# Kernel optimization log

Hardware: AMD Instinct MI355X
Metric: run time of the kernel (lower is better)

## Reference

```python
import jax, jax.numpy as jnp
import numpy as np

N = 100000
E = 1600000
IN_DIM = 64
HID = 64
OUT = 64
NCLS = 40
EPS_BN = 1e-5


def _sym_norms(src, dst, n):
    # DGL GraphConv norm='both': src scaled by out_degree^-1/2, dst by in_degree^-1/2,
    # degrees clamped to min 1.
    ones = jnp.ones(src.shape[0], dtype=jnp.float32)
    deg_out = jax.ops.segment_sum(ones, src, num_segments=n)
    deg_in = jax.ops.segment_sum(ones, dst, num_segments=n)
    return jnp.clip(deg_out, 1.0) ** -0.5, jnp.clip(deg_in, 1.0) ** -0.5


def _graph_conv(x, src, dst, norm_src, norm_dst, W, b):
    # D_dst^{-1/2} A D_src^{-1/2} X W + b
    x = x * norm_src[:, None]
    agg = jax.ops.segment_sum(x[src], dst, num_segments=x.shape[0])
    agg = agg * norm_dst[:, None]
    return agg @ W + b


def _gcn(x, src, dst, W1, b1, W2, b2):
    ns, nd = _sym_norms(src, dst, x.shape[0])
    h = jax.nn.relu(_graph_conv(x, src, dst, ns, nd, W1, b1))
    return _graph_conv(h, src, dst, ns, nd, W2, b2)


def setup_inputs() -> dict:
    key = jax.random.key(0)
    ks = jax.random.split(key, 16)
    glorot = lambda k, fi, fo: jax.random.normal(k, (fi, fo), jnp.float32) * np.sqrt(2.0 / (fi + fo))
    return {
        "feat1": jax.random.normal(ks[0], (N, IN_DIM), jnp.float32),
        "src1": jax.random.randint(ks[1], (E,), 0, N, jnp.int32),
        "dst1": jax.random.randint(ks[2], (E,), 0, N, jnp.int32),
        "feat2": jax.random.normal(ks[3], (N, IN_DIM), jnp.float32),
        "src2": jax.random.randint(ks[4], (E,), 0, N, jnp.int32),
        "dst2": jax.random.randint(ks[5], (E,), 0, N, jnp.int32),
        "W1a": glorot(ks[6], IN_DIM, HID), "b1a": jnp.zeros(HID, jnp.float32),
        "W1b": glorot(ks[7], HID, OUT), "b1b": jnp.zeros(OUT, jnp.float32),
        "W2a": glorot(ks[8], IN_DIM, HID), "b2a": jnp.zeros(HID, jnp.float32),
        "W2b": glorot(ks[9], HID, OUT), "b2b": jnp.zeros(OUT, jnp.float32),
        "Wm1": glorot(ks[10], OUT, HID), "bm1": jnp.zeros(HID, jnp.float32),
        "gamma": jnp.ones(HID, jnp.float32), "beta": jnp.zeros(HID, jnp.float32),
        "Wm2": glorot(ks[11], HID, NCLS), "bm2": jnp.zeros(NCLS, jnp.float32),
    }


def reference(feat1, src1, dst1, feat2, src2, dst2,
              W1a, b1a, W1b, b1b, W2a, b2a, W2b, b2b,
              Wm1, bm1, gamma, beta, Wm2, bm2):
    h1 = _gcn(feat1, src1, dst1, W1a, b1a, W1b, b1b)
    h2 = _gcn(feat2, src2, dst2, W2a, b2a, W2b, b2b)
    # torch .std() is unbiased (ddof=1)
    z1 = (h1 - h1.mean(0)) / jnp.std(h1, axis=0, ddof=1)
    z2 = (h2 - h2.mean(0)) / jnp.std(h2, axis=0, ddof=1)
    z = (z1 + z2) * 0.5
    # MLP2 head: Linear -> BatchNorm1d (training-mode batch stats) -> ReLU -> Linear
    y = z @ Wm1 + bm1
    mu = y.mean(0)
    var = y.var(0)  # biased, as BN uses
    y = (y - mu) * jax.lax.rsqrt(var + EPS_BN) * gamma + beta
    pred_y = jax.nn.relu(y) @ Wm2 + bm2
    return (z1, z2, pred_y)
```

## Files before the change

### kernel.cpp

```cpp
#include <hip/hip_runtime.h>
#include <hip/hip_bf16.h>

#define DIM 64
#define NCLS_OUT 40
#define BSH 8
#define BROWS 256
#define BIN_CHUNK 12288

typedef __hip_bfloat16 bf16;

__device__ __forceinline__ float lane_bcast(float v, int l) {
  return __int_as_float(__builtin_amdgcn_readlane(__float_as_int(v), l));
}
__device__ __forceinline__ unsigned short f2bf_bits(float f) {
  bf16 h = __float2bfloat16(f);
  return *reinterpret_cast<unsigned short*>(&h);
}

__device__ __forceinline__ float ldf(const void* p, long i, int m) {
  return m ? ((const float*)p)[i] : __bfloat162float(((const bf16*)p)[i]);
}
__device__ __forceinline__ void stf(void* p, long i, float v, int m) {
  if (m) ((float*)p)[i] = v;
  else ((bf16*)p)[i] = __float2bfloat16(v);
}

__global__ void k_detect(const unsigned int* __restrict__ wds, int nw, int* __restrict__ mode) {
  __shared__ int cnt_s;
  if (threadIdx.x == 0) cnt_s = 0;
  __syncthreads();
  int c = 0;
  for (int i = threadIdx.x; i < nw; i += 1024) {
    unsigned h = wds[i] & 0xFFFFu;
    unsigned e = (h >> 7) & 0xFFu;
    if (e == 0xFFu || (e != 0u && e < 0x60u)) c++;
  }
  atomicAdd(&cnt_s, c);
  __syncthreads();
  if (threadIdx.x == 0) *mode = (cnt_s > nw / 16) ? 1 : 0;
}

__global__ void k_deg_out(const int* __restrict__ src1, const int* __restrict__ src2,
                          int* __restrict__ deg, int n, int e1, int etot) {
  int i = blockIdx.x * 256 + threadIdx.x;
  if (i >= etot) return;
  if (i < e1) atomicAdd(&deg[2 * n + src1[i]], 1);
  else atomicAdd(&deg[3 * n + src2[i - e1]], 1);
}

__global__ void k_norm(const int* __restrict__ deg, float* __restrict__ nrm, int n4) {
  int i = blockIdx.x * 256 + threadIdx.x;
  if (i < n4) {
    int d = deg[i];
    if (d < 1) d = 1;
    nrm[i] = rsqrtf((float)d);
  }
}

__global__ void k_bhist(const int* __restrict__ dst1, const int* __restrict__ dst2,
                        int* __restrict__ bh, int n, int e1, int etot, int NB) {
  extern __shared__ int cnt[];
  for (int b = threadIdx.x; b < NB; b += blockDim.x) cnt[b] = 0;
  __syncthreads();
  int stride = gridDim.x * blockDim.x;
  for (int i = blockIdx.x * blockDim.x + threadIdx.x; i < etot; i += stride) {
    int row = (i < e1) ? dst1[i] : (n + dst2[i - e1]);
    atomicAdd(&cnt[row >> BSH], 1);
  }
  __syncthreads();
  for (int b = threadIdx.x; b < NB; b += blockDim.x)
    if (cnt[b]) atomicAdd(&bh[b], cnt[b]);
}

__global__ void k_bscan(const int* __restrict__ bh, int* __restrict__ bbase,
                        int* __restrict__ gcur, int* __restrict__ rp,
                        int NB, int etot, int n2) {
  __shared__ int sm[256];
  __shared__ int carry_s;
  int t = threadIdx.x;
  if (t == 0) carry_s = 0;
  __syncthreads();
  for (int base = 0; base < NB; base += 256) {
    int i = base + t;
    int v = (i < NB) ? bh[i] : 0;
    sm[t] = v;
    __syncthreads();
    for (int o = 1; o < 256; o <<= 1) {
      int a = (t >= o) ? sm[t - o] : 0;
      __syncthreads();
      sm[t] += a;
      __syncthreads();
    }
    int c = carry_s;
    int excl = c + sm[t] - v;
    int tot = sm[255];
    __syncthreads();
    if (i < NB) { bbase[i] = excl; gcur[i] = excl; }
    if (t == 0) carry_s = c + tot;
    __syncthreads();
  }
  if (t == 0) { bbase[NB] = etot; rp[n2] = etot; }
}

__global__ void __launch_bounds__(256) k_bin(
    const int* __restrict__ src1, const int* __restrict__ dst1,
    const int* __restrict__ src2, const int* __restrict__ dst2,
    int* __restrict__ gcur, unsigned* __restrict__ eb,
    int n, int e1, int etot, int NB) {
  extern __shared__ int lds[];
  int* cnt = lds;
  int* base = lds + NB;
  int t = threadIdx.x;
  int c0 = blockIdx.x * BIN_CHUNK;
  int cend = c0 + BIN_CHUNK;
  if (cend > etot) cend = etot;
  for (int b = t; b < NB; b += 256) cnt[b] = 0;
  __syncthreads();
  for (int i = c0 + t; i < cend; i += 256) {
    int row = (i < e1) ? dst1[i] : (n + dst2[i - e1]);
    atomicAdd(&cnt[row >> BSH], 1);
  }
  __syncthreads();
  for (int b = t; b < NB; b += 256) {
    int c = cnt[b];
    base[b] = c ? atomicAdd(&gcur[b], c) : 0;
    cnt[b] = 0;
  }
  __syncthreads();
  for (int i = c0 + t; i < cend; i += 256) {
    int s, row;
    if (i < e1) { s = src1[i]; row = dst1[i]; }
    else { s = src2[i - e1]; row = n + dst2[i - e1]; }
    int b = row >> BSH;
    int l = atomicAdd(&cnt[b], 1);
    eb[base[b] + l] = ((unsigned)(row & (BROWS - 1)) << 24) | (unsigned)s;
  }
}

__global__ void __launch_bounds__(256) k_fine(
    const unsigned* __restrict__ eb, const int* __restrict__ bbase,
    int* __restrict__ rp, int* __restrict__ deg, int* __restrict__ sb,
    int n2, int NB) {
  __shared__ int hist[256];
  __shared__ int sm[256];
  __shared__ int curs[256];
  int t = threadIdx.x;
  for (int b = blockIdx.x; b < NB; b += gridDim.x) {
    int ebeg = bbase[b], eend = bbase[b + 1];
    hist[t] = 0;
    __syncthreads();
    for (int i = ebeg + t; i < eend; i += 256)
      atomicAdd(&hist[eb[i] >> 24], 1);
    __syncthreads();
    int v = hist[t];
    sm[t] = v;
    __syncthreads();
    for (int o = 1; o < 256; o <<= 1) {
      int a = (t >= o) ? sm[t - o] : 0;
      __syncthreads();
      sm[t] += a;
      __syncthreads();
    }
    int excl = sm[t] - v;
    int row = (b << BSH) + t;
    if (row < n2) { deg[row] = v; rp[row] = ebeg + excl; }
    curs[t] = excl;
    __syncthreads();
    for (int i = ebeg + t; i < eend; i += 256) {
      unsigned u = eb[i];
      int l = atomicAdd(&curs[u >> 24], 1);
      sb[ebeg + l] = (int)(u & 0xFFFFFFu);
    }
    __syncthreads();
  }
}

__global__ void k_scale_all(const void* __restrict__ f1, const void* __restrict__ f2,
                            const float* __restrict__ norms, bf16* __restrict__ P,
                            int n, const int* __restrict__ mode) {
  int m = *mode;
  int i = blockIdx.x * 256 + threadIdx.x;
  int nd = n * DIM;
  if (i >= 2 * nd) return;
  int g = i >= nd;
  int li = g ? i - nd : i;
  float ns = norms[2 * n + g * n + (li >> 6)];
  P[i] = __float2bfloat16(ldf(g ? f2 : f1, li, m) * ns);
}

__global__ void k_scale_one(const void* __restrict__ f, const float* __restrict__ ns,
                            bf16* __restrict__ P, int nd, const int* __restrict__ mode) {
  int m = *mode;
  int i = blockIdx.x * 256 + threadIdx.x;
  if (i < nd) P[i] = __float2bfloat16(ldf(f, i, m) * ns[i >> 6]);
}

__global__ void __launch_bounds__(256) k_gmm(
    const bf16* __restrict__ X, const int* __restrict__ rp, const int* __restrict__ sb,
    const void* __restrict__ Wg0, const void* __restrict__ bg0,
    const void* __restrict__ Wg1, const void* __restrict__ bg1,
    const float* __restrict__ pre0, const float* __restrict__ pre1,
    const float* __restrict__ post0, const float* __restrict__ post1,
    bf16* __restrict__ Y, int n, int relu, const int* __restrict__ mode,
    int dual, int gsel, float* __restrict__ stats) {
  int m = *mode;
  int t = threadIdx.x, lane = t & 63, wid = t >> 6;
  int g = dual ? (blockIdx.x & 1) : gsel;
  int ord = dual ? (blockIdx.x >> 1) : blockIdx.x;
  int nblk = dual ? (gridDim.x >> 1) : gridDim.x;
  int rowbase = dual ? g * n : 0;

  const void* W = g ? Wg1 : Wg0;
  const void* bb = g ? bg1 : bg0;
  const float* pre = g ? pre1 : pre0;
  const float* post = g ? post1 : post0;

  unsigned wp[32];
#pragma unroll
  for (int i = 0; i < 32; ++i) {
    unsigned lb = f2bf_bits(ldf(W, (2 * i) * 64 + lane, m));
    unsigned hb = f2bf_bits(ldf(W, (2 * i + 1) * 64 + lane, m));
    wp[i] = lb | (hb << 16);
  }
  float bias = ldf(bb, lane, m);
  float ps = 0.f, pq = 0.f;

  int stride = nblk * 4;
  for (int node = ord * 4 + wid; node < n; node += stride) {
    int b0 = rp[g * n + node], e0 = rp[g * n + node + 1];
    float a0 = 0.f, a1 = 0.f, a2 = 0.f, a3 = 0.f;
    for (int base = b0; base < e0; base += 64) {
      int cnt = e0 - base;
      if (cnt > 64) cnt = 64;
      int eidx = (lane < cnt) ? sb[base + lane] : 0;
      int j = 0;
      for (; j + 8 <= cnt; j += 8) {
        int s0 = __builtin_amdgcn_readlane(eidx, j);
        int s1 = __builtin_amdgcn_readlane(eidx, j + 1);
        int s2 = __builtin_amdgcn_readlane(eidx, j + 2);
        int s3 = __builtin_amdgcn_readlane(eidx, j + 3);
        int s4 = __builtin_amdgcn_readlane(eidx, j + 4);
        int s5 = __builtin_amdgcn_readlane(eidx, j + 5);
        int s6 = __builtin_amdgcn_readlane(eidx, j + 6);
        int s7 = __builtin_amdgcn_readlane(eidx, j + 7);
        float v0 = __bfloat162float(X[(long)(rowbase + s0) * DIM + lane]);
        float v1 = __bfloat162float(X[(long)(rowbase + s1) * DIM + lane]);
        float v2 = __bfloat162float(X[(long)(rowbase + s2) * DIM + lane]);
        float v3 = __bfloat162float(X[(long)(rowbase + s3) * DIM + lane]);
        float v4 = __bfloat162float(X[(long)(rowbase + s4) * DIM + lane]);
        float v5 = __bfloat162float(X[(long)(rowbase + s5) * DIM + lane]);
        float v6 = __bfloat162float(X[(long)(rowbase + s6) * DIM + lane]);
        float v7 = __bfloat162float(X[(long)(rowbase + s7) * DIM + lane]);
        a0 += v0; a1 += v1; a2 += v2; a3 += v3;
        a0 += v4; a1 += v5; a2 += v6; a3 += v7;
      }
      for (; j + 4 <= cnt; j += 4) {
        int s0 = __builtin_amdgcn_readlane(eidx, j);
        int s1 = __builtin_amdgcn_readlane(eidx, j + 1);
        int s2 = __builtin_amdgcn_readlane(eidx, j + 2);
        int s3 = __builtin_amdgcn_readlane(eidx, j + 3);
        a0 += __bfloat162float(X[(long)(rowbase + s0) * DIM + lane]);
        a1 += __bfloat162float(X[(long)(rowbase + s1) * DIM + lane]);
        a2 += __bfloat162float(X[(long)(rowbase + s2) * DIM + lane]);
        a3 += __bfloat162float(X[(long)(rowbase + s3) * DIM + lane]);
      }
      for (; j < cnt; ++j) {
        int s0 = __builtin_amdgcn_readlane(eidx, j);
        a0 += __bfloat162float(X[(long)(rowbase + s0) * DIM + lane]);
      }
    }
    float acc = (a0 + a1) + (a2 + a3);
    acc *= pre[node];
    float r = 0.f;
#pragma unroll
    for (int i = 0; i < 32; ++i) {
      r = fmaf(lane_bcast(acc, 2 * i), __uint_as_float(wp[i] << 16), r);
      r = fmaf(lane_bcast(acc, 2 * i + 1), __uint_as_float(wp[i] & 0xFFFF0000u), r);
    }
    r += bias;
    if (relu) r = fmaxf(r, 0.f);
    if (post) r *= post[node];
    Y[(long)(rowbase + node) * DIM + lane] = __float2bfloat16(r);
    ps += r;
    pq += r * r;
  }

  if (stats) {
    __shared__ float ssum[4][64], ssq[4][64];
    ssum[wid][lane] = ps;
    ssq[wid][lane] = pq;
    __syncthreads();
    if (t < 64) {
      float a = ssum[0][t] + ssum[1][t] + ssum[2][t] + ssum[3][t];
      float b2 = ssq[0][t] + ssq[1][t] + ssq[2][t] + ssq[3][t];
      atomicAdd(&stats[g * 128 + t], a);
      atomicAdd(&stats[g * 128 + 64 + t], b2);
    }
  }
}

__global__ void __launch_bounds__(256) k_mm64s(const bf16* __restrict__ X,
                                               const void* __restrict__ W,
                                               const void* __restrict__ b,
                                               bf16* __restrict__ Y, int n,
                                               const int* __restrict__ mode,
                                               float* __restrict__ stats) {
  int m = *mode;
  int t = threadIdx.x, lane = t & 63, wid = t >> 6;
  float w[64];
#pragma unroll
  for (int k = 0; k < 64; ++k) w[k] = ldf(W, k * 64 + lane, m);
  float bias = ldf(b, lane, m);
  float ps = 0.f, pq = 0.f;
  int stride = gridDim.x * 4;
  for (int row = blockIdx.x * 4 + wid; row < n; row += stride) {
    float a = __bfloat162float(X[(long)row * 64 + lane]);
    float acc = 0.f;
#pragma unroll
    for (int k = 0; k < 64; ++k) acc = fmaf(lane_bcast(a, k), w[k], acc);
    acc += bias;
    Y[(long)row * 64 + lane] = __float2bfloat16(acc);
    ps += acc;
    pq += acc * acc;
  }
  __shared__ float ssum[4][64], ssq[4][64];
  ssum[wid][lane] = ps;
  ssq[wid][lane] = pq;
  __syncthreads();
  if (t < 64) {
    float a = ssum[0][t] + ssum[1][t] + ssum[2][t] + ssum[3][t];
    float b2 = ssq[0][t] + ssq[1][t] + ssq[2][t] + ssq[3][t];
    atomicAdd(&stats[t], a);
    atomicAdd(&stats[64 + t], b2);
  }
}

__global__ void k_z_dual(const bf16* __restrict__ H, const float* __restrict__ stats,
                         void* __restrict__ zout, bf16* __restrict__ Dz, int n,
                         const int* __restrict__ mode) {
  int m = *mode;
  int i = blockIdx.x * 256 + threadIdx.x;
  int nd = n * DIM;
  if (i >= nd) return;
  int c = i & 63;
  float fn = (float)n;
  float mu1 = stats[c] / fn;
  float var1 = fmaxf((stats[64 + c] - mu1 * mu1 * fn) / (fn - 1.0f), 1e-12f);
  float mu2 = stats[128 + c] / fn;
  float var2 = fmaxf((stats[192 + c] - mu2 * mu2 * fn) / (fn - 1.0f), 1e-12f);
  float z1 = (__bfloat162float(H[i]) - mu1) * rsqrtf(var1);
  float z2 = (__bfloat162float(H[nd + i]) - mu2) * rsqrtf(var2);
  stf(zout, i, z1, m);
  stf(zout, (long)nd + i, z2, m);
  Dz[i] = __float2bfloat16(0.5f * (z1 + z2));
}

__global__ void k_z_seq(const bf16* __restrict__ h, const float* __restrict__ stats,
                        void* __restrict__ zout, long zoff, bf16* __restrict__ zacc,
                        int n, int init, const int* __restrict__ mode) {
  int m = *mode;
  int i = blockIdx.x * 256 + threadIdx.x;
  if (i >= n * DIM) return;
  int c = i & 63;
  float fn = (float)n;
  float mu = stats[c] / fn;
  float var = fmaxf((stats[64 + c] - mu * mu * fn) / (fn - 1.0f), 1e-12f);
  float z = (__bfloat162float(h[i]) - mu) * rsqrtf(var);
  stf(zout, zoff + i, z, m);
  float prev = init ? 0.f : __bfloat162float(zacc[i]);
  zacc[i] = __float2bfloat16(prev + 0.5f * z);
}

__global__ void __launch_bounds__(256) k_head(const bf16* __restrict__ Yv,
                                              const float* __restrict__ s,
                                              const float* __restrict__ sq,
                                              const void* __restrict__ gamma,
                                              const void* __restrict__ beta,
                                              const void* __restrict__ W2,
                                              const void* __restrict__ b2,
                                              void* __restrict__ out, long ooff, int n,
                                              const int* __restrict__ mode) {
  int m = *mode;
  int t = threadIdx.x, lane = t & 63, wid = t >> 6;
  float w[64];
#pragma unroll
  for (int k = 0; k < 64; ++k)
    w[k] = (lane < NCLS_OUT) ? ldf(W2, k * NCLS_OUT + lane, m) : 0.f;
  float bias = (lane < NCLS_OUT) ? ldf(b2, lane, m) : 0.f;
  float fn = (float)n;
  float mu = s[lane] / fn;
  float var = sq[lane] / fn - mu * mu;
  float rstd = rsqrtf(fmaxf(var, 0.f) + 1e-5f);
  float g = ldf(gamma, lane, m);
  float be = ldf(beta, lane, m);
  int stride = gridDim.x * 4;
  for (int row = blockIdx.x * 4 + wid; row < n; row += stride) {
    float yv = __bfloat162float(Yv[(long)row * 64 + lane]);
    float yn = fmaxf((yv - mu) * rstd * g + be, 0.f);
    float acc = bias;
#pragma unroll
    for (int k = 0; k < 64; ++k) acc = fmaf(lane_bcast(yn, k), w[k], acc);
    if (lane < NCLS_OUT) stf(out, ooff + (long)row * NCLS_OUT + lane, acc, m);
  }
}

extern "C" void kernel_launch(void* const* d_in, const int* in_sizes, int n_in,
                              void* d_out, int out_size, void* d_ws, size_t ws_size,
                              hipStream_t stream) {
  const void* feat1 = d_in[0];
  const int* src1 = (const int*)d_in[1];
  const int* dst1 = (const int*)d_in[2];
  const void* feat2 = d_in[3];
  const int* src2 = (const int*)d_in[4];
  const int* dst2 = (const int*)d_in[5];
  const void* W1a = d_in[6];
  const void* b1a = d_in[7];
  const void* W1b = d_in[8];
  const void* b1b = d_in[9];
  const void* W2a = d_in[10];
  const void* b2a = d_in[11];
  const void* W2b = d_in[12];
  const void* b2b = d_in[13];
  const void* Wm1 = d_in[14];
  const void* bm1 = d_in[15];
  const void* gamma = d_in[16];
  const void* beta = d_in[17];
  const void* Wm2 = d_in[18];
  const void* bm2 = d_in[19];

  const int n = in_sizes[0] / DIM;
  const int e1 = in_sizes[1];
  const int e2 = in_sizes[4];
  const int etot = e1 + e2;
  const long nd = (long)n * DIM;
  const int NB = (2 * n + BROWS - 1) >> BSH;

  char* w = (char*)d_ws;
  size_t off = 0;
  auto alloc = [&](size_t bytes) -> void* {
    void* p = w + off;
    off += (bytes + 255) & ~(size_t)255;
    return p;
  };
  int* mode = (int*)alloc(256);
  int* deg = (int*)alloc((size_t)4 * n * 4);
  float* stats = (float*)alloc(512 * 4);
  float* norms = (float*)alloc((size_t)4 * n * 4);
  int* rp = (int*)alloc((size_t)(2 * n + 8) * 4);
  int* bh = (int*)alloc((size_t)(NB + 1) * 4);
  int* bbase = (int*)alloc((size_t)(NB + 1) * 4);
  int* gcur = (int*)alloc((size_t)(NB + 1) * 4);
  int* sb = (int*)alloc((size_t)etot * 4);
  size_t base_off = off;
  bool dual = (ws_size >= base_off + (size_t)5 * nd * 2 + 4096);

  bf16 *P, *Q, *Dz;
  size_t qbytes;
  if (dual) {
    P = (bf16*)alloc((size_t)2 * nd * 2);
    Q = (bf16*)alloc((size_t)2 * nd * 2);
    Dz = (bf16*)alloc((size_t)nd * 2);
    qbytes = (size_t)2 * nd * 2;
  } else {
    P = (bf16*)alloc((size_t)nd * 2);
    Q = (bf16*)alloc((size_t)nd * 2);
    Dz = (bf16*)alloc((size_t)nd * 2);
    qbytes = (size_t)nd * 2;
  }
  unsigned* eb = ((size_t)etot * 4 <= qbytes) ? (unsigned*)Q
                                              : (unsigned*)alloc((size_t)etot * 4);

  const float* nd1 = norms;
  const float* nd2 = norms + n;
  const float* ns1 = norms + 2 * n;
  const float* ns2 = norms + 3 * n;

  int gE = (etot + 255) / 256;
  int gND = (int)((nd + 255) / 256);
  int g2ND = (int)((2 * nd + 255) / 256);
  int g4N = (4 * n + 255) / 256;
  int gBIN = (etot + BIN_CHUNK - 1) / BIN_CHUNK;
  const int gGMM = 4096;

  hipMemsetAsync(deg + 2 * n, 0, (size_t)2 * n * 4, stream);
  hipMemsetAsync(stats, 0, 512 * 4, stream);
  hipMemsetAsync(bh, 0, (size_t)NB * 4, stream);

  k_detect<<<1, 1024, 0, stream>>>((const unsigned int*)feat1, 8192, mode);
  k_deg_out<<<gE, 256, 0, stream>>>(src1, src2, deg, n, e1, etot);

  k_bhist<<<256, 256, (size_t)NB * 4, stream>>>(dst1, dst2, bh, n, e1, etot, NB);
  k_bscan<<<1, 256, 0, stream>>>(bh, bbase, gcur, rp, NB, etot, 2 * n);
  k_bin<<<gBIN, 256, (size_t)2 * NB * 4, stream>>>(src1, dst1, src2, dst2, gcur, eb,
                                                   n, e1, etot, NB);
  k_fine<<<NB, 256, 0, stream>>>(eb, bbase, rp, deg, sb, 2 * n, NB);
  k_norm<<<g4N, 256, 0, stream>>>(deg, norms, 4 * n);

  if (dual) {
    k_scale_all<<<g2ND, 256, 0, stream>>>(feat1, feat2, norms, P, n, mode);
    k_gmm<<<gGMM, 256, 0, stream>>>(P, rp, sb, W1a, b1a, W2a, b2a, nd1, nd2, ns1, ns2,
                                    Q, n, 1, mode, 1, 0, (float*)nullptr);
    k_gmm<<<gGMM, 256, 0, stream>>>(Q, rp, sb, W1b, b1b, W2b, b2b, nd1, nd2,
                                    (const float*)nullptr, (const float*)nullptr,
                                    P, n, 0, mode, 1, 0, stats);
    k_z_dual<<<gND, 256, 0, stream>>>(P, stats, d_out, Dz, n, mode);
  } else {
    k_scale_one<<<gND, 256, 0, stream>>>(feat1, ns1, P, (int)nd, mode);
    k_gmm<<<gGMM, 256, 0, stream>>>(P, rp, sb, W1a, b1a, W1a, b1a, nd1, nd1, ns1, ns1,
                                    Q, n, 1, mode, 0, 0, (float*)nullptr);
    k_gmm<<<gGMM, 256, 0, stream>>>(Q, rp, sb, W1b, b1b, W1b, b1b, nd1, nd1,
                                    (const float*)nullptr, (const float*)nullptr,
                                    P, n, 0, mode, 0, 0, stats);
    k_z_seq<<<gND, 256, 0, stream>>>(P, stats, d_out, 0L, Dz, n, 1, mode);
    k_scale_one<<<gND, 256, 0, stream>>>(feat2, ns2, P, (int)nd, mode);
    k_gmm<<<gGMM, 256, 0, stream>>>(P, rp, sb, W2a, b2a, W2a, b2a, nd2, nd2, ns2, ns2,
                                    Q, n, 1, mode, 0, 1, (float*)nullptr);
    k_gmm<<<gGMM, 256, 0, stream>>>(Q, rp, sb, W2b, b2b, W2b, b2b, nd2, nd2,
                                    (const float*)nullptr, (const float*)nullptr,
                                    P, n, 0, mode, 0, 1, stats + 128);
    k_z_seq<<<gND, 256, 0, stream>>>(P, stats + 128, d_out, nd, Dz, n, 0, mode);
  }

  k_mm64s<<<512, 256, 0, stream>>>(Dz, Wm1, bm1, Q, n, mode, stats + 256);
  k_head<<<512, 256, 0, stream>>>(Q, stats + 256, stats + 320, gamma, beta, Wm2, bm2,
                                  d_out, 2 * nd, n, mode);
}
```

Before: 975.8 us.

## Gather four neighbor rows per load with 8-byte lanes in GCN aggregation

Changes the gather in the fused aggregate-and-matmul kernel so each wavefront fetches four neighbor rows at once: each 16-lane quarter loads one 128-byte bf16 row using 8-byte loads, replacing one 2-byte load per lane per neighbor. Partial sums are combined across quarters with xor shuffles, and the matmul broadcast is remapped to the new per-lane feature layout. It also prefetches the next node's row-pointer bounds to hide that latency. The aim is fewer, wider memory instructions for the irregular gather, at the cost of extra shuffles, select logic and tail masking.

Measured after the change: 1.025 ms. 1.05x slower.

```diff
diff --git a/kernel.cpp b/kernel.cpp
--- a/kernel.cpp
+++ b/kernel.cpp
@@ -205,10 +205,12 @@
     int dual, int gsel, float* __restrict__ stats) {
   int m = *mode;
   int t = threadIdx.x, lane = t & 63, wid = t >> 6;
+  int lo4 = lane & 15, q = lane >> 4;
   int g = dual ? (blockIdx.x & 1) : gsel;
   int ord = dual ? (blockIdx.x >> 1) : blockIdx.x;
   int nblk = dual ? (gridDim.x >> 1) : gridDim.x;
   int rowbase = dual ? g * n : 0;
+  const char* Xb = (const char*)X;
 
   const void* W = g ? Wg1 : Wg0;
   const void* bb = g ? bg1 : bg0;
@@ -226,56 +228,85 @@
   float ps = 0.f, pq = 0.f;
 
   int stride = nblk * 4;
-  for (int node = ord * 4 + wid; node < n; node += stride) {
-    int b0 = rp[g * n + node], e0 = rp[g * n + node + 1];
+  const int* rpg = rp + (long)g * n;
+  int node = ord * 4 + wid;
+  int b0 = 0, e0 = 0;
+  if (node < n) { b0 = rpg[node]; e0 = rpg[node + 1]; }
+  for (; node < n; node += stride) {
+    int nn = node + stride;
+    int nb0 = 0, ne0 = 0;
+    if (nn < n) { nb0 = rpg[nn]; ne0 = rpg[nn + 1]; }
     float a0 = 0.f, a1 = 0.f, a2 = 0.f, a3 = 0.f;
     for (int base = b0; base < e0; base += 64) {
       int cnt = e0 - base;
       if (cnt > 64) cnt = 64;
       int eidx = (lane < cnt) ? sb[base + lane] : 0;
-      int j = 0;
-      for (; j + 8 <= cnt; j += 8) {
-        int s0 = __builtin_amdgcn_readlane(eidx, j);
-        int s1 = __builtin_amdgcn_readlane(eidx, j + 1);
-        int s2 = __builtin_amdgcn_readlane(eidx, j + 2);
-        int s3 = __builtin_amdgcn_readlane(eidx, j + 3);
-        int s4 = __builtin_amdgcn_readlane(eidx, j + 4);
-        int s5 = __builtin_amdgcn_readlane(eidx, j + 5);
-        int s6 = __builtin_amdgcn_readlane(eidx, j + 6);
-        int s7 = __builtin_amdgcn_readlane(eidx, j + 7);
-        float v0 = __bfloat162float(X[(long)(rowbase + s0) * DIM + lane]);
-        float v1 = __bfloat162float(X[(long)(rowbase + s1) * DIM + lane]);
-        float v2 = __bfloat162float(X[(long)(rowbase + s2) * DIM + lane]);
-        float v3 = __bfloat162float(X[(long)(rowbase + s3) * DIM + lane]);
-        float v4 = __bfloat162float(X[(long)(rowbase + s4) * DIM + lane]);
-        float v5 = __bfloat162float(X[(long)(rowbase + s5) * DIM + lane]);
-        float v6 = __bfloat162float(X[(long)(rowbase + s6) * DIM + lane]);
-        float v7 = __bfloat162float(X[(long)(rowbase + s7) * DIM + lane]);
-        a0 += v0; a1 += v1; a2 += v2; a3 += v3;
-        a0 += v4; a1 += v5; a2 += v6; a3 += v7;
-      }
-      for (; j + 4 <= cnt; j += 4) {
-        int s0 = __builtin_amdgcn_readlane(eidx, j);
-        int s1 = __builtin_amdgcn_readlane(eidx, j + 1);
-        int s2 = __builtin_amdgcn_readlane(eidx, j + 2);
-        int s3 = __builtin_amdgcn_readlane(eidx, j + 3);
-        a0 += __bfloat162float(X[(long)(rowbase + s0) * DIM + lane]);
-        a1 += __bfloat162float(X[(long)(rowbase + s1) * DIM + lane]);
-        a2 += __bfloat162float(X[(long)(rowbase + s2) * DIM + lane]);
-        a3 += __bfloat162float(X[(long)(rowbase + s3) * DIM + lane]);
-      }
-      for (; j < cnt; ++j) {
-        int s0 = __builtin_amdgcn_readlane(eidx, j);
-        a0 += __bfloat162float(X[(long)(rowbase + s0) * DIM + lane]);
+      for (int j = 0; j < cnt; j += 16) {
+        int ge = cnt - j;
+        unsigned vx0 = 0, vy0 = 0, vx1 = 0, vy1 = 0;
+        unsigned vx2 = 0, vy2 = 0, vx3 = 0, vy3 = 0;
+#define GLOAD(G, VX, VY)                                                        \
+        if (4 * G + 4 <= ge) {                                                  \
+          int c0 = j + 4 * G;                                                   \
+          int sA = __builtin_amdgcn_readlane(eidx, c0);                         \
+          int sB = __builtin_amdgcn_readlane(eidx, c0 + 1);                     \
+          int sC = __builtin_amdgcn_readlane(eidx, c0 + 2);                     \
+          int sD = __builtin_amdgcn_readlane(eidx, c0 + 3);                     \
+          int sAB = (q & 1) ? sB : sA;                                          \
+          int sCD = (q & 1) ? sD : sC;                                          \
+          int s = (q & 2) ? sCD : sAB;                                          \
+          unsigned boff = ((unsigned)(rowbase + s) << 7) | (unsigned)(lo4 << 3);\
+          uint2 vv = *(const uint2*)(Xb + boff);                                \
+          VX = vv.x;                                                            \
+          VY = vv.y;                                                            \
+        } else if (4 * G < ge) {                                                \
+          int c0 = j + 4 * G;                                                   \
+          int cm = cnt - 1;                                                     \
+          int i1 = c0 + 1 > cm ? cm : c0 + 1;                                   \
+          int i2 = c0 + 2 > cm ? cm : c0 + 2;                                   \
+          int i3 = c0 + 3 > cm ? cm : c0 + 3;                                   \
+          int sA = __builtin_amdgcn_readlane(eidx, c0);                         \
+          int sB = __builtin_amdgcn_readlane(eidx, i1);                         \
+          int sC = __builtin_amdgcn_readlane(eidx, i2);                         \
+          int sD = __builtin_amdgcn_readlane(eidx, i3);                         \
+          int sAB = (q & 1) ? sB : sA;                                          \
+          int sCD = (q & 1) ? sD : sC;                                          \
+          int s = (q & 2) ? sCD : sAB;                                          \
+          unsigned boff = ((unsigned)(rowbase + s) << 7) | (unsigned)(lo4 << 3);\
+          uint2 vv = *(const uint2*)(Xb + boff);                                \
+          bool okv = (c0 + q) < cnt;                                            \
+          VX = okv ? vv.x : 0u;                                                 \
+          VY = okv ? vv.y : 0u;                                                 \
+        }
+        GLOAD(0, vx0, vy0)
+        GLOAD(1, vx1, vy1)
+        GLOAD(2, vx2, vy2)
+        GLOAD(3, vx3, vy3)
+#undef GLOAD
+        a0 += __uint_as_float(vx0 << 16); a1 += __uint_as_float(vx0 & 0xFFFF0000u);
+        a2 += __uint_as_float(vy0 << 16); a3 += __uint_as_float(vy0 & 0xFFFF0000u);
+        a0 += __uint_as_float(vx1 << 16); a1 += __uint_as_float(vx1 & 0xFFFF0000u);
+        a2 += __uint_as_float(vy1 << 16); a3 += __uint_as_float(vy1 & 0xFFFF0000u);
+        a0 += __uint_as_float(vx2 << 16); a1 += __uint_as_float(vx2 & 0xFFFF0000u);
+        a2 += __uint_as_float(vy2 << 16); a3 += __uint_as_float(vy2 & 0xFFFF0000u);
+        a0 += __uint_as_float(vx3 << 16); a1 += __uint_as_float(vx3 & 0xFFFF0000u);
+        a2 += __uint_as_float(vy3 << 16); a3 += __uint_as_float(vy3 & 0xFFFF0000u);
       }
     }
-    float acc = (a0 + a1) + (a2 + a3);
-    acc *= pre[node];
+    a0 += __shfl_xor(a0, 16); a1 += __shfl_xor(a1, 16);
+    a2 += __shfl_xor(a2, 16); a3 += __shfl_xor(a3, 16);
+    a0 += __shfl_xor(a0, 32); a1 += __shfl_xor(a1, 32);
+    a2 += __shfl_xor(a2, 32); a3 += __shfl_xor(a3, 32);
+    float pn = pre[node];
+    a0 *= pn; a1 *= pn; a2 *= pn; a3 *= pn;
     float r = 0.f;
 #pragma unroll
     for (int i = 0; i < 32; ++i) {
-      r = fmaf(lane_bcast(acc, 2 * i), __uint_as_float(wp[i] << 16), r);
-      r = fmaf(lane_bcast(acc, 2 * i + 1), __uint_as_float(wp[i] & 0xFFFF0000u), r);
+      int k0 = 2 * i, k1 = 2 * i + 1;
+      float s0 = ((k0 & 3) == 0) ? a0 : ((k0 & 3) == 1) ? a1 : ((k0 & 3) == 2) ? a2 : a3;
+      float s1 = ((k1 & 3) == 0) ? a0 : ((k1 & 3) == 1) ? a1 : ((k1 & 3) == 2) ? a2 : a3;
+      r = fmaf(lane_bcast(s0, k0 >> 2), __uint_as_float(wp[i] << 16), r);
+      r = fmaf(lane_bcast(s1, k1 >> 2), __uint_as_float(wp[i] & 0xFFFF0000u), r);
     }
     r += bias;
     if (relu) r = fmaxf(r, 0.f);
@@ -283,6 +314,7 @@
     Y[(long)(rowbase + node) * DIM + lane] = __float2bfloat16(r);
     ps += r;
     pq += r * r;
+    b0 = nb0; e0 = ne0;
   }
 
   if (stats) {
```

## Give each wave a contiguous node chunk with a double-buffered edge-stream gather

Applied to the files above, without the earlier changes.

The aggregation kernel now gives each wave a contiguous range of up to 16 destination nodes and walks their concatenated edge list in 32-edge batches. Batches are double-buffered in registers so the next batch's gathers are issued before the current one is summed. Per-node partial sums go to shared memory and are transformed by the 64x64 weight afterwards, and the grid size is now derived from the node count. This aims to hide gather latency and avoid the per-node tail loops, at the cost of more registers (64 buffered values) and 16KB of shared memory per block, which may lower occupancy.

Result: slower. 1.035 ms (+6.1%).

```diff
diff --git a/kernel.cpp b/kernel.cpp
--- a/kernel.cpp
+++ b/kernel.cpp
@@ -6,6 +6,7 @@
 #define BSH 8
 #define BROWS 256
 #define BIN_CHUNK 12288
+#define CHUNK_MAX 16
 
 typedef __hip_bfloat16 bf16;
 
@@ -203,12 +204,14 @@
     const float* __restrict__ post0, const float* __restrict__ post1,
     bf16* __restrict__ Y, int n, int relu, const int* __restrict__ mode,
     int dual, int gsel, float* __restrict__ stats) {
+  __shared__ float snap[4][CHUNK_MAX][64];
   int m = *mode;
   int t = threadIdx.x, lane = t & 63, wid = t >> 6;
   int g = dual ? (blockIdx.x & 1) : gsel;
   int ord = dual ? (blockIdx.x >> 1) : blockIdx.x;
   int nblk = dual ? (gridDim.x >> 1) : gridDim.x;
   int rowbase = dual ? g * n : 0;
+  const char* Xb = (const char*)X + ((long)rowbase << 7);
 
   const void* W = g ? Wg1 : Wg0;
   const void* bb = g ? bg1 : bg0;
@@ -225,64 +228,89 @@
   float bias = ldf(bb, lane, m);
   float ps = 0.f, pq = 0.f;
 
-  int stride = nblk * 4;
-  for (int node = ord * 4 + wid; node < n; node += stride) {
-    int b0 = rp[g * n + node], e0 = rp[g * n + node + 1];
-    float a0 = 0.f, a1 = 0.f, a2 = 0.f, a3 = 0.f;
-    for (int base = b0; base < e0; base += 64) {
-      int cnt = e0 - base;
-      if (cnt > 64) cnt = 64;
-      int eidx = (lane < cnt) ? sb[base + lane] : 0;
-      int j = 0;
-      for (; j + 8 <= cnt; j += 8) {
-        int s0 = __builtin_amdgcn_readlane(eidx, j);
-        int s1 = __builtin_amdgcn_readlane(eidx, j + 1);
-        int s2 = __builtin_amdgcn_readlane(eidx, j + 2);
-        int s3 = __builtin_amdgcn_readlane(eidx, j + 3);
-        int s4 = __builtin_amdgcn_readlane(eidx, j + 4);
-        int s5 = __builtin_amdgcn_readlane(eidx, j + 5);
-        int s6 = __builtin_amdgcn_readlane(eidx, j + 6);
-        int s7 = __builtin_amdgcn_readlane(eidx, j + 7);
-        float v0 = __bfloat162float(X[(long)(rowbase + s0) * DIM + lane]);
-        float v1 = __bfloat162float(X[(long)(rowbase + s1) * DIM + lane]);
-        float v2 = __bfloat162float(X[(long)(rowbase + s2) * DIM + lane]);
-        float v3 = __bfloat162float(X[(long)(rowbase + s3) * DIM + lane]);
-        float v4 = __bfloat162float(X[(long)(rowbase + s4) * DIM + lane]);
-        float v5 = __bfloat162float(X[(long)(rowbase + s5) * DIM + lane]);
-        float v6 = __bfloat162float(X[(long)(rowbase + s6) * DIM + lane]);
-        float v7 = __bfloat162float(X[(long)(rowbase + s7) * DIM + lane]);
-        a0 += v0; a1 += v1; a2 += v2; a3 += v3;
-        a0 += v4; a1 += v5; a2 += v6; a3 += v7;
-      }
-      for (; j + 4 <= cnt; j += 4) {
-        int s0 = __builtin_amdgcn_readlane(eidx, j);
-        int s1 = __builtin_amdgcn_readlane(eidx, j + 1);
-        int s2 = __builtin_amdgcn_readlane(eidx, j + 2);
-        int s3 = __builtin_amdgcn_readlane(eidx, j + 3);
-        a0 += __bfloat162float(X[(long)(rowbase + s0) * DIM + lane]);
-        a1 += __bfloat162float(X[(long)(rowbase + s1) * DIM + lane]);
-        a2 += __bfloat162float(X[(long)(rowbase + s2) * DIM + lane]);
-        a3 += __bfloat162float(X[(long)(rowbase + s3) * DIM + lane]);
-      }
-      for (; j < cnt; ++j) {
-        int s0 = __builtin_amdgcn_readlane(eidx, j);
-        a0 += __bfloat162float(X[(long)(rowbase + s0) * DIM + lane]);
+  int nwaves = nblk * 4;
+  int waveid = ord * 4 + wid;
+  int chunk = (n + nwaves - 1) / nwaves;
+  int n0 = waveid * chunk;
+  int n1 = n0 + chunk;
+  if (n1 > n) n1 = n;
+
+  if (n0 < n) {
+    const int* rpg = rp + (long)g * n;
+    int ri = n0 + lane;
+    if (ri > n) ri = n;
+    int rpv = rpg[ri];
+    int epos = __builtin_amdgcn_readlane(rpv, 0);
+    int eend = __builtin_amdgcn_readlane(rpv, n1 - n0);
+    int node = n0;
+    int nrel = 1;
+    int node_end = __builtin_amdgcn_readlane(rpv, nrel);
+    float acc = 0.f;
+
+#define SNAP_CLOSE()                                              \
+    { snap[wid][node - n0][lane] = acc; acc = 0.f;                \
+      node++; nrel++;                                             \
+      node_end = __builtin_amdgcn_readlane(rpv, nrel); }
+
+    while (node < n1 && node_end == epos) SNAP_CLOSE();
+
+#define ISSUE(VB, EI, REMV)                                                      \
+    { int li = lane & 31; if (li >= (REMV)) li = (REMV) - 1;                     \
+      int eidx = sb[(EI) + li];                                                  \
+      if ((REMV) == 32) {                                                        \
+        _Pragma("unroll") for (int k = 0; k < 32; ++k) {                         \
+          int s = __builtin_amdgcn_readlane(eidx, k);                            \
+          VB[k] = *(const unsigned short*)(Xb + ((long)s << 7) + (lane << 1));   \
+        }                                                                        \
+      } else {                                                                   \
+        _Pragma("unroll") for (int k = 0; k < 32; ++k) if (k < (REMV)) {         \
+          int s = __builtin_amdgcn_readlane(eidx, k);                            \
+          VB[k] = *(const unsigned short*)(Xb + ((long)s << 7) + (lane << 1));   \
+        }                                                                        \
+      } }
+
+#define CONSUME(VB, ES, REMV)                                                    \
+    { _Pragma("unroll") for (int k = 0; k < 32; ++k) if (k < (REMV)) {           \
+        acc += __uint_as_float((unsigned)VB[k] << 16);                           \
+        while (node < n1 && node_end == (ES) + k + 1) SNAP_CLOSE();              \
+      } }
+
+    unsigned short A[32], B[32];
+    int E = epos;
+    if (E < eend) {
+      int remA = eend - E; if (remA > 32) remA = 32;
+      int EA = E; ISSUE(A, EA, remA); E += remA;
+      int remB = 0, EB = 0;
+      for (;;) {
+        if (E < eend) { remB = eend - E; if (remB > 32) remB = 32; EB = E; ISSUE(B, EB, remB); E += remB; }
+        else remB = 0;
+        CONSUME(A, EA, remA);
+        if (!remB) break;
+        if (E < eend) { remA = eend - E; if (remA > 32) remA = 32; EA = E; ISSUE(A, EA, remA); E += remA; }
+        else remA = 0;
+        CONSUME(B, EB, remB);
+        if (!remA) break;
       }
     }
-    float acc = (a0 + a1) + (a2 + a3);
-    acc *= pre[node];
-    float r = 0.f;
+#undef SNAP_CLOSE
+#undef ISSUE
+#undef CONSUME
+
+    for (int dn = n0; dn < n1; ++dn) {
+      float a = snap[wid][dn - n0][lane] * pre[dn];
+      float r = 0.f;
 #pragma unroll
-    for (int i = 0; i < 32; ++i) {
-      r = fmaf(lane_bcast(acc, 2 * i), __uint_as_float(wp[i] << 16), r);
-      r = fmaf(lane_bcast(acc, 2 * i + 1), __uint_as_float(wp[i] & 0xFFFF0000u), r);
+      for (int i = 0; i < 32; ++i) {
+        r = fmaf(lane_bcast(a, 2 * i), __uint_as_float(wp[i] << 16), r);
+        r = fmaf(lane_bcast(a, 2 * i + 1), __uint_as_float(wp[i] & 0xFFFF0000u), r);
+      }
+      r += bias;
+      if (relu) r = fmaxf(r, 0.f);
+      if (post) r *= post[dn];
+      Y[((long)rowbase + dn) * DIM + lane] = __float2bfloat16(r);
+      ps += r;
+      pq += r * r;
     }
-    r += bias;
-    if (relu) r = fmaxf(r, 0.f);
-    if (post) r *= post[node];
-    Y[(long)(rowbase + node) * DIM + lane] = __float2bfloat16(r);
-    ps += r;
-    pq += r * r;
   }
 
   if (stats) {
@@ -480,7 +508,10 @@
   int g2ND = (int)((2 * nd + 255) / 256);
   int g4N = (4 * n + 255) / 256;
   int gBIN = (etot + BIN_CHUNK - 1) / BIN_CHUNK;
-  const int gGMM = 4096;
+  int wavesPerGraph = (n + CHUNK_MAX - 1) / CHUNK_MAX;
+  int blkPerGraph = (wavesPerGraph + 3) / 4;
+  int gGMM_dual = 2 * blkPerGraph;
+  int gGMM_one = blkPerGraph;
 
   hipMemsetAsync(deg + 2 * n, 0, (size_t)2 * n * 4, stream);
   hipMemsetAsync(stats, 0, 512 * 4, stream);
@@ -498,26 +529,26 @@
 
   if (dual) {
     k_scale_all<<<g2ND, 256, 0, stream>>>(feat1, feat2, norms, P, n, mode);
-    k_gmm<<<gGMM, 256, 0, stream>>>(P, rp, sb, W1a, b1a, W2a, b2a, nd1, nd2, ns1, ns2,
-                                    Q, n, 1, mode, 1, 0, (float*)nullptr);
-    k_gmm<<<gGMM, 256, 0, stream>>>(Q, rp, sb, W1b, b1b, W2b, b2b, nd1, nd2,
-                                    (const float*)nullptr, (const float*)nullptr,
-                                    P, n, 0, mode, 1, 0, stats);
+    k_gmm<<<gGMM_dual, 256, 0, stream>>>(P, rp, sb, W1a, b1a, W2a, b2a, nd1, nd2, ns1, ns2,
+                                         Q, n, 1, mode, 1, 0, (float*)nullptr);
+    k_gmm<<<gGMM_dual, 256, 0, stream>>>(Q, rp, sb, W1b, b1b, W2b, b2b, nd1, nd2,
+                                         (const float*)nullptr, (const float*)nullptr,
+                                         P, n, 0, mode, 1, 0, stats);
     k_z_dual<<<gND, 256, 0, stream>>>(P, stats, d_out, Dz, n, mode);
   } else {
     k_scale_one<<<gND, 256, 0, stream>>>(feat1, ns1, P, (int)nd, mode);
-    k_gmm<<<gGMM, 256, 0, stream>>>(P, rp, sb, W1a, b1a, W1a, b1a, nd1, nd1, ns1, ns1,
-                                    Q, n, 1, mode, 0, 0, (float*)nullptr);
-    k_gmm<<<gGMM, 256, 0, stream>>>(Q, rp, sb, W1b, b1b, W1b, b1b, nd1, nd1,
-                                    (const float*)nullptr, (const float*)nullptr,
-                                    P, n, 0, mode, 0, 0, stats);
+    k_gmm<<<gGMM_one, 256, 0, stream>>>(P, rp, sb, W1a, b1a, W1a, b1a, nd1, nd1, ns1, ns1,
+                                        Q, n, 1, mode, 0, 0, (float*)nullptr);
+    k_gmm<<<gGMM_one, 256, 0, stream>>>(Q, rp, sb, W1b, b1b, W1b, b1b, nd1, nd1,
+                                        (const float*)nullptr, (const float*)nullptr,
+                                        P, n, 0, mode, 0, 0, stats);
     k_z_seq<<<gND, 256, 0, stream>>>(P, stats, d_out, 0L, Dz, n, 1, mode);
     k_scale_one<<<gND, 256, 0, stream>>>(feat2, ns2, P, (int)nd, mode);
-    k_gmm<<<gGMM, 256, 0, stream>>>(P, rp, sb, W2a, b2a, W2a, b2a, nd2, nd2, ns2, ns2,
-                                    Q, n, 1, mode, 0, 1, (float*)nullptr);
-    k_gmm<<<gGMM, 256, 0, stream>>>(Q, rp, sb, W2b, b2b, W2b, b2b, nd2, nd2,
-                                    (const float*)nullptr, (const float*)nullptr,
-                                    P, n, 0, mode, 0, 1, stats + 128);
+    k_gmm<<<gGMM_one, 256, 0, stream>>>(P, rp, sb, W2a, b2a, W2a, b2a, nd2, nd2, ns2, ns2,
+                                        Q, n, 1, mode, 0, 1, (float*)nullptr);
+    k_gmm<<<gGMM_one, 256, 0, stream>>>(Q, rp, sb, W2b, b2b, W2b, b2b, nd2, nd2,
+                                        (const float*)nullptr, (const float*)nullptr,
+                                        P, n, 0, mode, 0, 1, stats + 128);
     k_z_seq<<<gND, 256, 0, stream>>>(P, stats + 128, d_out, nd, Dz, n, 0, mode);
   }
 
```

## Gather neighbor rows with per-lane 128-bit loads staged through swizzled LDS

Applied to the files above, without the earlier changes.

The aggregation loop in k_gmm used to issue one 2-byte load per lane per neighbor row, with the index taken by readlane. Now each lane loads a whole 128-byte neighbor row as eight uint4 loads into a per-wave XOR-swizzled LDS buffer, and the wave then reads its column back from LDS. The row-pointer values for the next node are also prefetched one iteration early. This replaces many narrow, latency-bound gathers with wide vector loads, at the cost of 32KB of LDS per block (lower occupancy) and extra LDS traffic.

After: 1.075 ms. +10.2%, slower.

```diff
diff --git a/kernel.cpp b/kernel.cpp
--- a/kernel.cpp
+++ b/kernel.cpp
@@ -203,12 +203,15 @@
     const float* __restrict__ post0, const float* __restrict__ post1,
     bf16* __restrict__ Y, int n, int relu, const int* __restrict__ mode,
     int dual, int gsel, float* __restrict__ stats) {
+  __shared__ __align__(16) char xs[4][8192];
   int m = *mode;
   int t = threadIdx.x, lane = t & 63, wid = t >> 6;
   int g = dual ? (blockIdx.x & 1) : gsel;
   int ord = dual ? (blockIdx.x >> 1) : blockIdx.x;
   int nblk = dual ? (gridDim.x >> 1) : gridDim.x;
   int rowbase = dual ? g * n : 0;
+  const char* Xb = (const char*)X + ((long)rowbase << 7);
+  char* xsw = xs[wid];
 
   const void* W = g ? Wg1 : Wg0;
   const void* bb = g ? bg1 : bg0;
@@ -225,49 +228,42 @@
   float bias = ldf(bb, lane, m);
   float ps = 0.f, pq = 0.f;
 
+  int swz = lane & 7;
   int stride = nblk * 4;
-  for (int node = ord * 4 + wid; node < n; node += stride) {
-    int b0 = rp[g * n + node], e0 = rp[g * n + node + 1];
+  const int* rpg = rp + (long)g * n;
+  int node = ord * 4 + wid;
+  int b0 = 0, e0 = 0;
+  if (node < n) { b0 = rpg[node]; e0 = rpg[node + 1]; }
+  for (; node < n; node += stride) {
+    int nn = node + stride;
+    int nb0 = 0, ne0 = 0;
+    if (nn < n) { nb0 = rpg[nn]; ne0 = rpg[nn + 1]; }
     float a0 = 0.f, a1 = 0.f, a2 = 0.f, a3 = 0.f;
     for (int base = b0; base < e0; base += 64) {
       int cnt = e0 - base;
       if (cnt > 64) cnt = 64;
-      int eidx = (lane < cnt) ? sb[base + lane] : 0;
+      int li = (lane < cnt) ? lane : 0;
+      int eidx = sb[base + li];
+      const uint4* rowp = (const uint4*)(Xb + ((long)eidx << 7));
+      uint4 r0 = rowp[0], r1 = rowp[1], r2 = rowp[2], r3 = rowp[3];
+      uint4 r4 = rowp[4], r5 = rowp[5], r6 = rowp[6], r7 = rowp[7];
+      uint4* wrow = (uint4*)(xsw + lane * 128);
+      wrow[0 ^ swz] = r0; wrow[1 ^ swz] = r1;
+      wrow[2 ^ swz] = r2; wrow[3 ^ swz] = r3;
+      wrow[4 ^ swz] = r4; wrow[5 ^ swz] = r5;
+      wrow[6 ^ swz] = r6; wrow[7 ^ swz] = r7;
+#define RD(J, K) __uint_as_float((unsigned)(*(const unsigned short*)(             \
+        xsw + ((J) + (K)) * 128 + ((lane << 1) ^ ((K) << 4)))) << 16)
       int j = 0;
       for (; j + 8 <= cnt; j += 8) {
-        int s0 = __builtin_amdgcn_readlane(eidx, j);
-        int s1 = __builtin_amdgcn_readlane(eidx, j + 1);
-        int s2 = __builtin_amdgcn_readlane(eidx, j + 2);
-        int s3 = __builtin_amdgcn_readlane(eidx, j + 3);
-        int s4 = __builtin_amdgcn_readlane(eidx, j + 4);
-        int s5 = __builtin_amdgcn_readlane(eidx, j + 5);
-        int s6 = __builtin_amdgcn_readlane(eidx, j + 6);
-        int s7 = __builtin_amdgcn_readlane(eidx, j + 7);
-        float v0 = __bfloat162float(X[(long)(rowbase + s0) * DIM + lane]);
-        float v1 = __bfloat162float(X[(long)(rowbase + s1) * DIM + lane]);
-        float v2 = __bfloat162float(X[(long)(rowbase + s2) * DIM + lane]);
-        float v3 = __bfloat162float(X[(long)(rowbase + s3) * DIM + lane]);
-        float v4 = __bfloat162float(X[(long)(rowbase + s4) * DIM + lane]);
-        float v5 = __bfloat162float(X[(long)(rowbase + s5) * DIM + lane]);
-        float v6 = __bfloat162float(X[(long)(rowbase + s6) * DIM + lane]);
-        float v7 = __bfloat162float(X[(long)(rowbase + s7) * DIM + lane]);
-        a0 += v0; a1 += v1; a2 += v2; a3 += v3;
-        a0 += v4; a1 += v5; a2 += v6; a3 += v7;
-      }
-      for (; j + 4 <= cnt; j += 4) {
-        int s0 = __builtin_amdgcn_readlane(eidx, j);
-        int s1 = __builtin_amdgcn_readlane(eidx, j + 1);
-        int s2 = __builtin_amdgcn_readlane(eidx, j + 2);
-        int s3 = __builtin_amdgcn_readlane(eidx, j + 3);
-        a0 += __bfloat162float(X[(long)(rowbase + s0) * DIM + lane]);
-        a1 += __bfloat162float(X[(long)(rowbase + s1) * DIM + lane]);
-        a2 += __bfloat162float(X[(long)(rowbase + s2) * DIM + lane]);
-        a3 += __bfloat162float(X[(long)(rowbase + s3) * DIM + lane]);
+        a0 += RD(j, 0); a1 += RD(j, 1); a2 += RD(j, 2); a3 += RD(j, 3);
+        a0 += RD(j, 4); a1 += RD(j, 5); a2 += RD(j, 6); a3 += RD(j, 7);
       }
       for (; j < cnt; ++j) {
-        int s0 = __builtin_amdgcn_readlane(eidx, j);
-        a0 += __bfloat162float(X[(long)(rowbase + s0) * DIM + lane]);
+        a0 += __uint_as_float((unsigned)(*(const unsigned short*)(
+            xsw + j * 128 + ((lane << 1) ^ ((j & 7) << 4)))) << 16);
       }
+#undef RD
     }
     float acc = (a0 + a1) + (a2 + a3);
     acc *= pre[node];
@@ -283,16 +279,19 @@
     Y[(long)(rowbase + node) * DIM + lane] = __float2bfloat16(r);
     ps += r;
     pq += r * r;
+    b0 = nb0; e0 = ne0;
   }
 
   if (stats) {
-    __shared__ float ssum[4][64], ssq[4][64];
-    ssum[wid][lane] = ps;
-    ssq[wid][lane] = pq;
+    __syncthreads();
+    float* ssum = (float*)xs;
+    float* ssq = ssum + 256;
+    ssum[wid * 64 + lane] = ps;
+    ssq[wid * 64 + lane] = pq;
     __syncthreads();
     if (t < 64) {
-      float a = ssum[0][t] + ssum[1][t] + ssum[2][t] + ssum[3][t];
-      float b2 = ssq[0][t] + ssq[1][t] + ssq[2][t] + ssq[3][t];
+      float a = ssum[t] + ssum[64 + t] + ssum[128 + t] + ssum[192 + t];
+      float b2 = ssq[t] + ssq[64 + t] + ssq[128 + t] + ssq[192 + t];
       atomicAdd(&stats[g * 128 + t], a);
       atomicAdd(&stats[g * 128 + 64 + t], b2);
     }
```
